# Kernel tuning notes

Hardware: AMD Instinct MI355X
Metric: run time of the kernel (lower is better)

The kernel has to match this reference:

```python
import jax, jax.numpy as jnp
import numpy as np

D_MODEL = 1024
NUM_HEADS = 16
D_K = D_MODEL // NUM_HEADS  # 64
THETA = 10000.0


def apply_rope(x, positions, theta):
    # x: [b, h, s, d_k]; interleaved-pair RoPE
    d = x.shape[-1]
    inv_freq = theta ** (-jnp.arange(0, d, 2, dtype=jnp.float32) / d)  # [d/2]
    angles = positions.astype(jnp.float32)[:, None] * inv_freq[None, :]  # [s, d/2]
    cos = jnp.cos(angles)
    sin = jnp.sin(angles)
    x1 = x[..., 0::2]
    x2 = x[..., 1::2]
    out_even = x1 * cos - x2 * sin
    out_odd = x1 * sin + x2 * cos
    return jnp.stack([out_even, out_odd], axis=-1).reshape(x.shape)


def setup_inputs() -> dict:
    key = jax.random.key(0)
    kx, kq, kk, kv, ko = jax.random.split(key, 5)
    scale = 1.0 / np.sqrt(D_MODEL)
    return {
        "x": jax.random.normal(kx, (1, 4096, D_MODEL), dtype=jnp.float32),
        "Wq": jax.random.normal(kq, (D_MODEL, D_MODEL), dtype=jnp.float32) * scale,
        "Wk": jax.random.normal(kk, (D_MODEL, D_MODEL), dtype=jnp.float32) * scale,
        "Wv": jax.random.normal(kv, (D_MODEL, D_MODEL), dtype=jnp.float32) * scale,
        "Wo": jax.random.normal(ko, (D_MODEL, D_MODEL), dtype=jnp.float32) * scale,
    }


def reference(x, Wq, Wk, Wv, Wo):
    b, s, _ = x.shape
    # Linear (no bias, weight stored as [out, in]): y = x @ W^T
    q = jnp.einsum("bsd,ed->bse", x, Wq).reshape(b, s, NUM_HEADS, D_K).transpose(0, 2, 1, 3)
    k = jnp.einsum("bsd,ed->bse", x, Wk).reshape(b, s, NUM_HEADS, D_K).transpose(0, 2, 1, 3)
    v = jnp.einsum("bsd,ed->bse", x, Wv).reshape(b, s, NUM_HEADS, D_K).transpose(0, 2, 1, 3)

    positions = jnp.arange(s)
    q = apply_rope(q, positions, THETA)
    k = apply_rope(k, positions, THETA)

    scores = jnp.einsum("bhqd,bhkd->bhqk", q, k) / jnp.sqrt(jnp.float32(D_K))
    causal = jnp.tril(jnp.ones((s, s), dtype=bool))
    scores = jnp.where(causal, scores, -jnp.inf)
    probs = jax.nn.softmax(scores, axis=-1)
    ctx = jnp.einsum("bhqk,bhkd->bhqd", probs, v)  # [b,h,s,d_k]
    ctx = ctx.transpose(0, 2, 1, 3).reshape(b, s, D_MODEL)
    return jnp.einsum("bse,de->bsd", ctx, Wo)
```

## Files before the change

### kernel.cpp

```cpp
#include <hip/hip_runtime.h>
#include <hip/hip_bf16.h>
#include <math.h>


#define S_LEN 4096
#define DMODEL 1024
#define NHEAD 16
#define QSCALE 0.1803368801111244f
#define PSTR 76

typedef __attribute__((ext_vector_type(8))) short short8;
typedef __attribute__((ext_vector_type(4))) short short4_t;
typedef __attribute__((ext_vector_type(2))) unsigned int uint2_t;
typedef __attribute__((ext_vector_type(4))) unsigned int uint4_t;
typedef __attribute__((ext_vector_type(4))) float floatx4;

static __device__ __forceinline__ void load_lds16(const void* g, void* l) {
    __builtin_amdgcn_global_load_lds((const __attribute__((address_space(1))) void*)g,
                                     (__attribute__((address_space(3))) void*)l, 16, 0, 0);
}

static __device__ __forceinline__ __hip_bfloat16 bf16_fast(float f) {
    unsigned int u = __builtin_bit_cast(unsigned int, f) + 0x8000u;
    unsigned short s = (unsigned short)(u >> 16);
    return __builtin_bit_cast(__hip_bfloat16, s);
}
static __device__ __forceinline__ unsigned int pack_bf16x2(float a, float b) {
    unsigned int ua = __builtin_bit_cast(unsigned int, a) + 0x8000u;
    unsigned int ub = __builtin_bit_cast(unsigned int, b) + 0x8000u;
    return __builtin_amdgcn_perm(ub, ua, 0x07060302);
}

__global__ void cvt_all_kernel(const float* __restrict__ x,  const float* __restrict__ wq,
                               const float* __restrict__ wk, const float* __restrict__ wv,
                               const float* __restrict__ wo,
                               __hip_bfloat16* __restrict__ xb,  __hip_bfloat16* __restrict__ wqb,
                               __hip_bfloat16* __restrict__ wkb, __hip_bfloat16* __restrict__ wvb,
                               __hip_bfloat16* __restrict__ wob)
{
    const size_t NX = (size_t)S_LEN * DMODEL;
    const size_t NW = (size_t)DMODEL * DMODEL;
    size_t t = ((size_t)blockIdx.x * blockDim.x + threadIdx.x) * 8;
    const float* src; __hip_bfloat16* dst; size_t off;
    if (t < NX) { src = x; dst = xb; off = t; }
    else {
        size_t j = t - NX; int seg = (int)(j >> 20); off = j & (NW - 1);
        src = (seg == 0) ? wq : (seg == 1) ? wk : (seg == 2) ? wv : wo;
        dst = (seg == 0) ? wqb : (seg == 1) ? wkb : (seg == 2) ? wvb : wob;
    }
    int row = (int)(off >> 10);
    int k   = (int)(off & 1023);
    int gp  = (((k >> 3) ^ row) & 7);
    size_t doff = (off & ~(size_t)1023) + (size_t)((k & ~63) + (gp << 3));
    float4 v0 = *(const float4*)(src + off);
    float4 v1 = *(const float4*)(src + off + 4);
    uint4_t w;
    w.x = pack_bf16x2(v0.x, v0.y);
    w.y = pack_bf16x2(v0.z, v0.w);
    w.z = pack_bf16x2(v1.x, v1.y);
    w.w = pack_bf16x2(v1.z, v1.w);
    *(uint4_t*)(dst + doff) = w;
}

__global__ __launch_bounds__(256) void qkv_gemm(
    const __hip_bfloat16* __restrict__ A,
    const __hip_bfloat16* __restrict__ Bq,
    const __hip_bfloat16* __restrict__ Bk,
    const __hip_bfloat16* __restrict__ Bv,
    __hip_bfloat16* __restrict__ Qb,
    __hip_bfloat16* __restrict__ Kb,
    __hip_bfloat16* __restrict__ Vtb)
{
    __shared__ __hip_bfloat16 As[128 * 64];
    __shared__ __hip_bfloat16 Bs[128 * 64];
    const int tid  = threadIdx.x;
    const int wave = tid >> 6;
    const int lane = tid & 63;
    const int quad = lane >> 4;
    const int l15  = lane & 15;
    const int k7   = l15 & 7;
    const int sec  = blockIdx.x >> 3;
    const __hip_bfloat16* B = (sec == 0) ? Bq : (sec == 1) ? Bk : Bv;
    const int n0 = (blockIdx.x & 7) * 128;
    const int m0 = blockIdx.y * 128;
    const int wm = (wave & 1) * 64;
    const int wn = (wave >> 1) * 64;

    floatx4 acc[4][4] = {};

    for (int kt = 0; kt < DMODEL; kt += 64) {
        #pragma unroll
        for (int p = 0; p < 8; ++p) {
            int id  = p * 4 + wave;
            int cb  = (id & 15) * 1024;
            int bb  = cb + lane * 16;
            int row = bb >> 7;
            int ce  = (bb & 127) >> 1;
            if (id < 16)
                load_lds16(A + (size_t)(m0 + row) * DMODEL + kt + ce, (char*)As + cb);
            else
                load_lds16(B + (size_t)(n0 + row) * DMODEL + kt + ce, (char*)Bs + cb);
        }
        __syncthreads();
        #pragma unroll
        for (int dc = 0; dc < 2; ++dc) {
            short8 af[4], bf[4];
            #pragma unroll
            for (int i = 0; i < 4; ++i)
                af[i] = *(const short8*)(As + (wm + i * 16 + l15) * 64 + (((dc * 4 + quad) ^ k7) << 3));
            #pragma unroll
            for (int j = 0; j < 4; ++j)
                bf[j] = *(const short8*)(Bs + (wn + j * 16 + l15) * 64 + (((dc * 4 + quad) ^ k7) << 3));
            #pragma unroll
            for (int i = 0; i < 4; ++i)
                #pragma unroll
                for (int j = 0; j < 4; ++j)
                    acc[i][j] = __builtin_amdgcn_mfma_f32_16x16x32_bf16(af[i], bf[j], acc[i][j], 0, 0, 0);
        }
        __syncthreads();
    }

    float ifreq[4];
    #pragma unroll
    for (int j = 0; j < 4; ++j) {
        int d = (j * 16 + l15) & 63;
        ifreq[j] = expf(-(float)(d & ~1) * (9.210340371976184f / 64.0f));
    }
    const float scale = (sec == 0) ? QSCALE : 1.0f;
    __hip_bfloat16* dst = (sec == 0) ? Qb : Kb;
    #pragma unroll
    for (int i = 0; i < 4; ++i) {
        int rowb = m0 + wm + i * 16 + quad * 4;
        #pragma unroll
        for (int j = 0; j < 4; ++j) {
            int col = n0 + wn + j * 16 + l15;
            int h   = col >> 6;
            int hd  = col & 63;
            if (sec == 2) {
                uint2_t w;
                w.x = pack_bf16x2(acc[i][j][0], acc[i][j][1]);
                w.y = pack_bf16x2(acc[i][j][2], acc[i][j][3]);
                int od = hd >> 4, lv = hd & 15;
                *(uint2_t*)(Vtb + (size_t)h * 262144 +
                            (((od * 512 + (rowb >> 3)) * 16 + lv) << 3) + (rowb & 7)) = w;
            } else {
                int g = hd >> 3, jj = hd & 7;
                #pragma unroll
                for (int r = 0; r < 4; ++r) {
                    int rr  = rowb + r;
                    float v = acc[i][j][r];
                    float ang = (float)rr * ifreq[j];
                    float sn, cs;
                    __sincosf(ang, &sn, &cs);
                    float pv  = __shfl_xor(v, 1);
                    float out = ((lane & 1) ? (pv * sn + v * cs)
                                            : (v * cs - pv * sn)) * scale;
                    dst[(size_t)h * 262144 +
                        ((((rr >> 4) * 8 + g) * 16 + (rr & 15)) << 3) + jj] = bf16_fast(out);
                }
            }
        }
    }
}

template<bool EDGE>
static __device__ __forceinline__ void attn_tile(
    int kt, int quad, int l15,
    const __hip_bfloat16* __restrict__ Kh, const __hip_bfloat16* __restrict__ Vh,
    const short8 aq[4][2], floatx4 o[4][4], float lp[4],
    __hip_bfloat16* __restrict__ PsW)
{
    asm volatile("s_waitcnt lgkmcnt(0)" ::: "memory");

    short8 kf[4][2], vf[4][2];
    #pragma unroll
    for (int ni = 0; ni < 4; ++ni)
        #pragma unroll
        for (int dc = 0; dc < 2; ++dc)
            kf[ni][dc] = *(const short8*)(Kh + (size_t)(((((kt*4 + ni)*8 + dc*4 + quad)*16 + l15) << 3)));
    #pragma unroll
    for (int od = 0; od < 4; ++od)
        #pragma unroll
        for (int dc = 0; dc < 2; ++dc)
            vf[od][dc] = *(const short8*)(Vh + (size_t)((((od*512 + kt*8 + dc*4 + quad)*16 + l15) << 3)));

    #pragma unroll
    for (int g = 0; g < 4; ++g) {
        __hip_bfloat16* strip = PsW + (g * 16 + l15) * PSTR;
        floatx4 st[4];
        #pragma unroll
        for (int ni = 0; ni < 4; ++ni) {
            floatx4 z = {};
            floatx4 s = __builtin_amdgcn_mfma_f32_16x16x32_bf16(kf[ni][0], aq[g][0], z, 0, 0, 0);
            st[ni]    = __builtin_amdgcn_mfma_f32_16x16x32_bf16(kf[ni][1], aq[g][1], s, 0, 0, 0);
        }
        #pragma unroll
        for (int ni = 0; ni < 4; ++ni) {
            float e[4];
            #pragma unroll
            for (int r = 0; r < 4; ++r) {
                float v = __builtin_amdgcn_exp2f(st[ni][r]);
                if (EDGE) {
                    if (ni * 16 + quad * 4 + r > g * 16 + l15) v = 0.0f;
                }
                e[r] = v;
            }
            lp[g] += (e[0] + e[1]) + (e[2] + e[3]);
            uint2_t w;
            w.x = pack_bf16x2(e[0], e[1]);
            w.y = pack_bf16x2(e[2], e[3]);
            *(short4_t*)(strip + ni * 16 + quad * 4) = __builtin_bit_cast(short4_t, w);
        }
        short8 ap[2];
        #pragma unroll
        for (int dc = 0; dc < 2; ++dc) {
            const __hip_bfloat16* pp = strip + dc * 32 + quad * 8;
            short4_t p0 = *(const short4_t*)pp;
            short4_t p1 = *(const short4_t*)(pp + 4);
            short8 a;
            a[0] = p0[0]; a[1] = p0[1]; a[2] = p0[2]; a[3] = p0[3];
            a[4] = p1[0]; a[5] = p1[1]; a[6] = p1[2]; a[7] = p1[3];
            ap[dc] = a;
        }
        #pragma unroll
        for (int od = 0; od < 4; ++od) {
            o[g][od] = __builtin_amdgcn_mfma_f32_16x16x32_bf16(ap[0], vf[od][0], o[g][od], 0, 0, 0);
            o[g][od] = __builtin_amdgcn_mfma_f32_16x16x32_bf16(ap[1], vf[od][1], o[g][od], 0, 0, 0);
        }
    }
}

__global__ __launch_bounds__(256, 2) void attn_kernel(
    const __hip_bfloat16* __restrict__ Q,
    const __hip_bfloat16* __restrict__ Kp,
    const __hip_bfloat16* __restrict__ Vp,
    __hip_bfloat16* __restrict__ CTX)
{
    __shared__ __hip_bfloat16 Buf[4][64 * PSTR];
    __shared__ float LPw[4][64];
    const int b  = blockIdx.x;
    const int h  = b & 15;
    const int u  = 63 - (b >> 4);
    const int tid  = threadIdx.x;
    const int wave = tid >> 6, lane = tid & 63;
    const int quad = lane >> 4, l15 = lane & 15;

    const __hip_bfloat16* Qh = Q  + (size_t)h * 262144;
    const __hip_bfloat16* Kh = Kp + (size_t)h * 262144;
    const __hip_bfloat16* Vh = Vp + (size_t)h * 262144;
    __hip_bfloat16* PsW = &Buf[wave][0];

    short8 aq[4][2];
    #pragma unroll
    for (int g = 0; g < 4; ++g)
        #pragma unroll
        for (int dc = 0; dc < 2; ++dc)
            aq[g][dc] = *(const short8*)(Qh + (size_t)(((((u*4 + g)*8 + dc*4 + quad)*16 + l15) << 3)));

    floatx4 o[4][4] = {};
    float lp[4] = {};

    for (int kt = wave; kt < u; kt += 4)
        attn_tile<false>(kt, quad, l15, Kh, Vh, aq, o, lp, PsW);
    if ((u & 3) == wave)
        attn_tile<true>(u, quad, l15, Kh, Vh, aq, o, lp, PsW);

    #pragma unroll
    for (int g = 0; g < 4; ++g) {
        float v = lp[g];
        v += __shfl_xor(v, 16);
        v += __shfl_xor(v, 32);
        lp[g] = v;
    }
    asm volatile("s_waitcnt lgkmcnt(0)" ::: "memory");
    if (quad == 0) {
        #pragma unroll
        for (int g = 0; g < 4; ++g)
            LPw[wave][g * 16 + l15] = lp[g];
    }
    #pragma unroll
    for (int g = 0; g < 4; ++g)
        #pragma unroll
        for (int od = 0; od < 4; ++od)
            #pragma unroll
            for (int r = 0; r < 4; ++r)
                Buf[wave][(g * 16 + quad * 4 + r) * PSTR + od * 16 + l15] =
                    bf16_fast(o[g][od][r]);
    __syncthreads();

    #pragma unroll
    for (int r = 0; r < 4; ++r) {
        int q   = wave * 16 + quad * 4 + r;
        int row = u * 64 + q;
        float ls = LPw[0][q] + LPw[1][q] + LPw[2][q] + LPw[3][q];
        float rl = __frcp_rn(ls);
        #pragma unroll
        for (int od = 0; od < 4; ++od) {
            float s = 0.0f;
            #pragma unroll
            for (int sl = 0; sl < 4; ++sl)
                s += __bfloat162float(Buf[sl][q * PSTR + od * 16 + l15]);
            int cidx = od * 16 + l15;
            int gp   = (((cidx >> 3) ^ row) & 7);
            CTX[(size_t)row * DMODEL + h * 64 + (gp << 3) + (cidx & 7)] =
                bf16_fast(s * rl);
        }
    }
}

__global__ __launch_bounds__(256) void out_gemm(
    const __hip_bfloat16* __restrict__ A,
    const __hip_bfloat16* __restrict__ B,
    float* __restrict__ C)
{
    __shared__ __hip_bfloat16 As[128 * 64];
    __shared__ __hip_bfloat16 Bs[64 * 64];
    const int tid  = threadIdx.x;
    const int wave = tid >> 6;
    const int lane = tid & 63;
    const int quad = lane >> 4;
    const int l15  = lane & 15;
    const int k7   = l15 & 7;
    const int n0 = blockIdx.x * 64;
    const int m0 = blockIdx.y * 128;
    const int wm = (wave & 1) * 64;
    const int wn = (wave >> 1) * 32;

    floatx4 acc[4][2] = {};

    for (int kt = 0; kt < DMODEL; kt += 64) {
        #pragma unroll
        for (int p = 0; p < 6; ++p) {
            int id  = p * 4 + wave;
            if (id < 16) {
                int cb  = id * 1024;
                int bb  = cb + lane * 16;
                int row = bb >> 7;
                int ce  = (bb & 127) >> 1;
                load_lds16(A + (size_t)(m0 + row) * DMODEL + kt + ce, (char*)As + cb);
            } else {
                int cb  = (id - 16) * 1024;
                int bb  = cb + lane * 16;
                int row = bb >> 7;
                int ce  = (bb & 127) >> 1;
                load_lds16(B + (size_t)(n0 + row) * DMODEL + kt + ce, (char*)Bs + cb);
            }
        }
        __syncthreads();
        #pragma unroll
        for (int dc = 0; dc < 2; ++dc) {
            short8 af[4], bf[2];
            #pragma unroll
            for (int i = 0; i < 4; ++i)
                af[i] = *(const short8*)(As + (wm + i * 16 + l15) * 64 + (((dc * 4 + quad) ^ k7) << 3));
            #pragma unroll
            for (int j = 0; j < 2; ++j)
                bf[j] = *(const short8*)(Bs + (wn + j * 16 + l15) * 64 + (((dc * 4 + quad) ^ k7) << 3));
            #pragma unroll
            for (int i = 0; i < 4; ++i)
                #pragma unroll
                for (int j = 0; j < 2; ++j)
                    acc[i][j] = __builtin_amdgcn_mfma_f32_16x16x32_bf16(af[i], bf[j], acc[i][j], 0, 0, 0);
        }
        __syncthreads();
    }

    #pragma unroll
    for (int i = 0; i < 4; ++i) {
        int rowb = m0 + wm + i * 16 + quad * 4;
        #pragma unroll
        for (int j = 0; j < 2; ++j) {
            int col = n0 + wn + j * 16 + l15;
            #pragma unroll
            for (int r = 0; r < 4; ++r)
                C[(size_t)(rowb + r) * DMODEL + col] = acc[i][j][r];
        }
    }
}

extern "C" void kernel_launch(void* const* d_in, const int* in_sizes, int n_in,
                              void* d_out, int out_size, void* d_ws, size_t ws_size,
                              hipStream_t stream)
{
    const float* x  = (const float*)d_in[0];
    const float* Wq = (const float*)d_in[1];
    const float* Wk = (const float*)d_in[2];
    const float* Wv = (const float*)d_in[3];
    const float* Wo = (const float*)d_in[4];

    char* ws = (char*)d_ws;
    const size_t MB = 1024 * 1024;
    __hip_bfloat16* xb  = (__hip_bfloat16*)(ws);
    __hip_bfloat16* wqb = (__hip_bfloat16*)(ws +  8 * MB);
    __hip_bfloat16* wkb = (__hip_bfloat16*)(ws + 10 * MB);
    __hip_bfloat16* wvb = (__hip_bfloat16*)(ws + 12 * MB);
    __hip_bfloat16* wob = (__hip_bfloat16*)(ws + 14 * MB);
    __hip_bfloat16* Qb  = (__hip_bfloat16*)(ws + 16 * MB);
    __hip_bfloat16* Kbf = (__hip_bfloat16*)(ws + 24 * MB);
    __hip_bfloat16* Vtb = (__hip_bfloat16*)(ws + 32 * MB);
    __hip_bfloat16* Cx  = (__hip_bfloat16*)(ws + 40 * MB);

    cvt_all_kernel<<<4096, 256, 0, stream>>>(x, Wq, Wk, Wv, Wo, xb, wqb, wkb, wvb, wob);

    qkv_gemm<<<dim3(24, 32), 256, 0, stream>>>(xb, wqb, wkb, wvb, Qb, Kbf, Vtb);

    attn_kernel<<<1024, 256, 0, stream>>>(Qb, Kbf, Vtb, Cx);

    out_gemm<<<dim3(16, 32), 256, 0, stream>>>(Cx, wob, (float*)d_out);
}
```

Measured before the change: 189.3 us.

## Pair causal query tiles per block and reduce partials with LDS atomics

Each 512-thread block now handles two query tiles per head, u and 63-u, in two groups of four waves. This balances the causal triangle workload across blocks and halves the grid. Per-wave partial outputs and row sums are accumulated into fp32 LDS buffers with atomicAdd, replacing the bf16 staging followed by a 4-way sum. The per-wave P strip shrinks to 16 rows, and the lgkmcnt wait moves to just before the P stores. The LDS atomics and the zero-initialisation add cost, and the launch bounds now request 4 blocks of 512 threads, which raises register pressure.

```diff
diff --git a/kernel.cpp b/kernel.cpp
--- a/kernel.cpp
+++ b/kernel.cpp
@@ -168,10 +168,8 @@
     int kt, int quad, int l15,
     const __hip_bfloat16* __restrict__ Kh, const __hip_bfloat16* __restrict__ Vh,
     const short8 aq[4][2], floatx4 o[4][4], float lp[4],
-    __hip_bfloat16* __restrict__ PsW)
-{
-    asm volatile("s_waitcnt lgkmcnt(0)" ::: "memory");
-
+    __hip_bfloat16* __restrict__ strip)
+{
     short8 kf[4][2], vf[4][2];
     #pragma unroll
     for (int ni = 0; ni < 4; ++ni)
@@ -186,7 +184,7 @@
 
     #pragma unroll
     for (int g = 0; g < 4; ++g) {
-        __hip_bfloat16* strip = PsW + (g * 16 + l15) * PSTR;
+        __hip_bfloat16* srow = strip + l15 * PSTR;
         floatx4 st[4];
         #pragma unroll
         for (int ni = 0; ni < 4; ++ni) {
@@ -194,27 +192,31 @@
             floatx4 s = __builtin_amdgcn_mfma_f32_16x16x32_bf16(kf[ni][0], aq[g][0], z, 0, 0, 0);
             st[ni]    = __builtin_amdgcn_mfma_f32_16x16x32_bf16(kf[ni][1], aq[g][1], s, 0, 0, 0);
         }
+        float e[4][4];
         #pragma unroll
         for (int ni = 0; ni < 4; ++ni) {
-            float e[4];
             #pragma unroll
             for (int r = 0; r < 4; ++r) {
                 float v = __builtin_amdgcn_exp2f(st[ni][r]);
                 if (EDGE) {
                     if (ni * 16 + quad * 4 + r > g * 16 + l15) v = 0.0f;
                 }
-                e[r] = v;
+                e[ni][r] = v;
             }
-            lp[g] += (e[0] + e[1]) + (e[2] + e[3]);
+            lp[g] += (e[ni][0] + e[ni][1]) + (e[ni][2] + e[ni][3]);
+        }
+        asm volatile("s_waitcnt lgkmcnt(0)" ::: "memory");
+        #pragma unroll
+        for (int ni = 0; ni < 4; ++ni) {
             uint2_t w;
-            w.x = pack_bf16x2(e[0], e[1]);
-            w.y = pack_bf16x2(e[2], e[3]);
-            *(short4_t*)(strip + ni * 16 + quad * 4) = __builtin_bit_cast(short4_t, w);
+            w.x = pack_bf16x2(e[ni][0], e[ni][1]);
+            w.y = pack_bf16x2(e[ni][2], e[ni][3]);
+            *(short4_t*)(srow + ni * 16 + quad * 4) = __builtin_bit_cast(short4_t, w);
         }
         short8 ap[2];
         #pragma unroll
         for (int dc = 0; dc < 2; ++dc) {
-            const __hip_bfloat16* pp = strip + dc * 32 + quad * 8;
+            const __hip_bfloat16* pp = srow + dc * 32 + quad * 8;
             short4_t p0 = *(const short4_t*)pp;
             short4_t p1 = *(const short4_t*)(pp + 4);
             short8 a;
@@ -230,25 +232,36 @@
     }
 }
 
-__global__ __launch_bounds__(256, 2) void attn_kernel(
+__global__ __launch_bounds__(512, 4) void attn_kernel(
     const __hip_bfloat16* __restrict__ Q,
     const __hip_bfloat16* __restrict__ Kp,
     const __hip_bfloat16* __restrict__ Vp,
     __hip_bfloat16* __restrict__ CTX)
 {
-    __shared__ __hip_bfloat16 Buf[4][64 * PSTR];
-    __shared__ float LPw[4][64];
-    const int b  = blockIdx.x;
-    const int h  = b & 15;
-    const int u  = 63 - (b >> 4);
+    __shared__ __hip_bfloat16 Ps[8][16 * PSTR];
+    __shared__ float Obuf[2][64][68];
+    __shared__ float LPf[2][64];
+    const int b   = blockIdx.x;
+    const int h   = b & 15;
+    const int j   = b >> 4;
     const int tid  = threadIdx.x;
-    const int wave = tid >> 6, lane = tid & 63;
+    const int wave = tid >> 6;
+    const int grp  = wave >> 2;
+    const int w4   = wave & 3;
+    const int u    = grp ? j : 63 - j;
+    const int lane = tid & 63;
     const int quad = lane >> 4, l15 = lane & 15;
+
+    {
+        float* zb = &Obuf[0][0][0];
+        for (int i = tid; i < 2 * 64 * 68; i += 512) zb[i] = 0.0f;
+        if (tid < 128) LPf[tid >> 6][tid & 63] = 0.0f;
+    }
 
     const __hip_bfloat16* Qh = Q  + (size_t)h * 262144;
     const __hip_bfloat16* Kh = Kp + (size_t)h * 262144;
     const __hip_bfloat16* Vh = Vp + (size_t)h * 262144;
-    __hip_bfloat16* PsW = &Buf[wave][0];
+    __hip_bfloat16* strip = &Ps[wave][0];
 
     short8 aq[4][2];
     #pragma unroll
@@ -260,10 +273,12 @@
     floatx4 o[4][4] = {};
     float lp[4] = {};
 
-    for (int kt = wave; kt < u; kt += 4)
-        attn_tile<false>(kt, quad, l15, Kh, Vh, aq, o, lp, PsW);
-    if ((u & 3) == wave)
-        attn_tile<true>(u, quad, l15, Kh, Vh, aq, o, lp, PsW);
+    for (int kt = w4; kt < u; kt += 4)
+        attn_tile<false>(kt, quad, l15, Kh, Vh, aq, o, lp, strip);
+    if ((u & 3) == w4)
+        attn_tile<true>(u, quad, l15, Kh, Vh, aq, o, lp, strip);
+
+    __syncthreads();
 
     #pragma unroll
     for (int g = 0; g < 4; ++g) {
@@ -272,11 +287,10 @@
         v += __shfl_xor(v, 32);
         lp[g] = v;
     }
-    asm volatile("s_waitcnt lgkmcnt(0)" ::: "memory");
     if (quad == 0) {
         #pragma unroll
         for (int g = 0; g < 4; ++g)
-            LPw[wave][g * 16 + l15] = lp[g];
+            atomicAdd(&LPf[grp][g * 16 + l15], lp[g]);
     }
     #pragma unroll
     for (int g = 0; g < 4; ++g)
@@ -284,22 +298,17 @@
         for (int od = 0; od < 4; ++od)
             #pragma unroll
             for (int r = 0; r < 4; ++r)
-                Buf[wave][(g * 16 + quad * 4 + r) * PSTR + od * 16 + l15] =
-                    bf16_fast(o[g][od][r]);
+                atomicAdd(&Obuf[grp][g * 16 + quad * 4 + r][od * 16 + l15], o[g][od][r]);
     __syncthreads();
 
     #pragma unroll
     for (int r = 0; r < 4; ++r) {
-        int q   = wave * 16 + quad * 4 + r;
+        int q   = w4 * 16 + quad * 4 + r;
         int row = u * 64 + q;
-        float ls = LPw[0][q] + LPw[1][q] + LPw[2][q] + LPw[3][q];
-        float rl = __frcp_rn(ls);
+        float rl = __frcp_rn(LPf[grp][q]);
         #pragma unroll
         for (int od = 0; od < 4; ++od) {
-            float s = 0.0f;
-            #pragma unroll
-            for (int sl = 0; sl < 4; ++sl)
-                s += __bfloat162float(Buf[sl][q * PSTR + od * 16 + l15]);
+            float s  = Obuf[grp][q][od * 16 + l15];
             int cidx = od * 16 + l15;
             int gp   = (((cidx >> 3) ^ row) & 7);
             CTX[(size_t)row * DMODEL + h * 64 + (gp << 3) + (cidx & 7)] =
@@ -404,7 +413,7 @@
 
     qkv_gemm<<<dim3(24, 32), 256, 0, stream>>>(xb, wqb, wkb, wvb, Qb, Kbf, Vtb);
 
-    attn_kernel<<<1024, 256, 0, stream>>>(Qb, Kbf, Vtb, Cx);
+    attn_kernel<<<512, 512, 0, stream>>>(Qb, Kbf, Vtb, Cx);
 
     out_gemm<<<dim3(16, 32), 256, 0, stream>>>(Cx, wob, (float*)d_out);
 }
```

Result: slower. 445.5 us (+135.3%).
